# Optimization experiments

Hardware: AMD Instinct MI355X
Metric: run time of the kernel (lower is better)

## Reference

```python
import jax, jax.numpy as jnp
import numpy as np

EPS_L2 = 1e-6
EPS_RMS = 1e-6

def _dw_causal(x, w):
    # depthwise causal conv: x [B,L,C], w [C,K] (torch Conv1d weight [C,1,K] squeezed)
    K = w.shape[1]
    L = x.shape[1]
    xp = jnp.pad(x, ((0, 0), (K - 1, 0), (0, 0)))
    out = jnp.zeros_like(x)
    for j in range(K):  # K=4, fixed small kernel
        out = out + w[:, j] * xp[:, j:j + L, :]
    return out

def _qkv_conv(x, dw, pw):
    # depthwise causal conv -> pointwise 1x1 conv -> SiLU
    return jax.nn.silu(_dw_causal(x, dw) @ pw.T)

def _l2n(x):
    return x / (jnp.linalg.norm(x, axis=-1, keepdims=True) + EPS_L2)

def setup_inputs() -> dict:
    key = jax.random.key(0)
    B, L, D, M, P, K = 2, 1024, 2048, 2048, 8, 4
    ks = jax.random.split(key, 16)
    inp = {}
    inp['x'] = jax.random.normal(ks[0], (B, L, D), dtype=jnp.float32)
    inp['Wq'] = jax.random.normal(ks[1], (M, D), dtype=jnp.float32) * 0.02
    inp['Wk'] = jax.random.normal(ks[2], (M, D), dtype=jnp.float32) * 0.02
    inp['Wv'] = jax.random.normal(ks[3], (M, D), dtype=jnp.float32) * 0.02
    inp['q_dw'] = jax.random.normal(ks[4], (M, K), dtype=jnp.float32) * 0.1
    inp['k_dw'] = jax.random.normal(ks[5], (M, K), dtype=jnp.float32) * 0.1
    inp['v_dw'] = jax.random.normal(ks[6], (M, K), dtype=jnp.float32) * 0.1
    inp['q_pw'] = jax.random.normal(ks[7], (M, M), dtype=jnp.float32) * 0.02
    inp['k_pw'] = jax.random.normal(ks[8], (M, M), dtype=jnp.float32) * 0.02
    inp['v_pw'] = jax.random.normal(ks[9], (M, M), dtype=jnp.float32) * 0.02
    inp['pk'] = jax.random.normal(ks[10], (P, M), dtype=jnp.float32) * 0.02
    inp['pv'] = jax.random.normal(ks[11], (P, M), dtype=jnp.float32) * 0.02
    inp['mlp_w1'] = jnp.eye(M, dtype=jnp.float32) * 0.1
    inp['mlp_w2'] = jnp.eye(M, dtype=jnp.float32) * 0.1
    inp['eta_w'] = jnp.zeros((1, D), dtype=jnp.float32)
    inp['eta_b'] = jnp.full((1,), 2.0, dtype=jnp.float32)
    inp['theta_w'] = jnp.zeros((1, D), dtype=jnp.float32)
    inp['theta_b'] = jnp.full((1,), -1.0, dtype=jnp.float32)
    inp['alpha_w'] = jnp.zeros((1, D), dtype=jnp.float32)
    inp['alpha_b'] = jnp.full((1,), -2.0, dtype=jnp.float32)
    inp['gate_w'] = jax.random.normal(ks[12], (M, M), dtype=jnp.float32) * 0.02
    inp['gate_b'] = jnp.zeros((M,), dtype=jnp.float32)
    inp['out_w'] = jax.random.normal(ks[13], (D, M), dtype=jnp.float32) * 0.02
    inp['ln_w'] = jnp.ones((D,), dtype=jnp.float32)
    inp['mem_state'] = jnp.zeros((M, M), dtype=jnp.float32)
    inp['sur_state'] = jnp.zeros((M, M), dtype=jnp.float32)
    return inp

def reference(x, Wq, Wk, Wv, q_dw, q_pw, k_dw, k_pw, v_dw, v_pw, pk, pv,
              mlp_w1, mlp_w2, eta_w, eta_b, theta_w, theta_b, alpha_w, alpha_b,
              gate_w, gate_b, out_w, ln_w, mem_state, sur_state):
    B, L, D = x.shape
    M = Wq.shape[0]
    P = pk.shape[0]
    # projections + causal depthwise-separable convs + SiLU
    q = _qkv_conv(x @ Wq.T, q_dw, q_pw)
    k = _qkv_conv(x @ Wk.T, k_dw, k_pw)
    v = _qkv_conv(x @ Wv.T, v_dw, v_pw)
    q = _l2n(q)
    k = _l2n(k)
    # data-dependent eta/theta/alpha from mean-pooled input, scalarized
    x_pooled = x.mean(axis=1)  # [B, D]
    eta = jax.nn.sigmoid(x_pooled @ eta_w.T + eta_b).mean()
    theta = jax.nn.sigmoid(x_pooled @ theta_w.T + theta_b).mean()
    alpha = jax.nn.sigmoid(x_pooled @ alpha_w.T + alpha_b).mean()
    # persistent memory tokens
    pk_n = _l2n(pk)
    k_wp = jnp.concatenate([jnp.broadcast_to(pk_n[None], (B, P, M)), k], axis=1)
    v_wp = jnp.concatenate([jnp.broadcast_to(pv[None], (B, P, M)), v], axis=1)
    # test-time memory update (torch.no_grad block -> stop_gradient)
    pred = jnp.einsum('blm,mh->blh', k, mem_state)
    err = v - pred
    momentary = jnp.einsum('bld,blh->dh', k, err) / (B * L)
    new_surprise = eta * sur_state + theta * momentary
    new_memory = (1.0 - alpha) * mem_state + new_surprise
    snapshot = jax.lax.stop_gradient(new_memory)
    # retrieval: linear memory + deep memory MLP
    linear_ret = jnp.einsum('blm,mh->blh', q, snapshot)
    mlp_ret = jax.nn.silu(q @ mlp_w1.T) @ mlp_w2.T
    retrieved = linear_ret + mlp_ret
    # causal attention with always-visible persistent tokens
    scores = jnp.einsum('blm,bpm->blp', q, k_wp) / jnp.sqrt(jnp.float32(M))
    col = jnp.arange(P + L)
    row = jnp.arange(L)
    mask = (col[None, :] < P) | ((col[None, :] - P) <= row[:, None])  # [L, P+L]
    scores = jnp.where(mask[None], scores, -jnp.inf)
    attn = jax.nn.softmax(scores.astype(jnp.float32), axis=-1).astype(x.dtype)
    context = jnp.einsum('blp,bpm->blm', attn, v_wp)
    retrieved = retrieved + context
    # gated output projection + residual + RMSNorm
    gate = jax.nn.sigmoid(retrieved @ gate_w.T + gate_b)
    out = x + (gate * retrieved) @ out_w.T
    rms = jnp.sqrt(jnp.mean(out * out, axis=-1, keepdims=True) + EPS_RMS)
    return (out / rms) * ln_w
```

## Files before the change

kernel.cpp:

```cpp
#include <hip/hip_runtime.h>
#include <hip/hip_bf16.h>


#define NROWS 2048
#define MD    2048
#define PL    1032
#define PLP   1152
#define NM    4194304

using bf16x8 = __attribute__((ext_vector_type(8))) __bf16;
using f32x4  = __attribute__((ext_vector_type(4))) float;
using u16x8  = __attribute__((ext_vector_type(8))) unsigned short;

__device__ __forceinline__ unsigned short f2bf(float f) {
    union { float f; unsigned int u; } c; c.f = f;
    unsigned int u = c.u;
    return (unsigned short)((u + 0x7fffu + ((u >> 16) & 1u)) >> 16);
}
__device__ __forceinline__ float bf2f(unsigned short h) {
    union { float f; unsigned int u; } c; c.u = ((unsigned int)h) << 16;
    return c.f;
}
__device__ __forceinline__ float ldf(const float* p) { return *p; }
__device__ __forceinline__ float ldf(const unsigned short* p) { return bf2f(*p); }
__device__ __forceinline__ float sigm(float x) { return 1.f / (1.f + __expf(-x)); }
__device__ __forceinline__ float silu(float x) { return x / (1.f + __expf(-x)); }

__device__ __forceinline__ float block_reduce_sum(float v) {
    __shared__ float ws[4];
    #pragma unroll
    for (int o = 32; o > 0; o >>= 1) v += __shfl_down(v, o);
    __syncthreads();
    if ((threadIdx.x & 63) == 0) ws[threadIdx.x >> 6] = v;
    __syncthreads();
    return (ws[0] + ws[1]) + (ws[2] + ws[3]);
}
__device__ __forceinline__ float block_reduce_max(float v) {
    __shared__ float wm[4];
    #pragma unroll
    for (int o = 32; o > 0; o >>= 1) v = fmaxf(v, __shfl_down(v, o));
    __syncthreads();
    if ((threadIdx.x & 63) == 0) wm[threadIdx.x >> 6] = v;
    __syncthreads();
    return fmaxf(fmaxf(wm[0], wm[1]), fmaxf(wm[2], wm[3]));
}

__device__ __forceinline__ void load_lds16(const unsigned short* g, unsigned short* l) {
    __builtin_amdgcn_global_load_lds(
        (const __attribute__((address_space(1))) unsigned int*)g,
        (__attribute__((address_space(3))) unsigned int*)l, 16, 0, 0);
}
__device__ __forceinline__ void raw_barrier() {
    __asm__ volatile("" ::: "memory");
    __builtin_amdgcn_s_barrier();
    __asm__ volatile("" ::: "memory");
}
__device__ __forceinline__ void epi_store(int epi, float* Cf, unsigned short* Ch,
                                          long off, float v) {
    if (epi == 0)      Cf[off] = v;
    else if (epi == 1) Cf[off] += v;
    else if (epi == 2) Ch[off] = f2bf(v);
    else               Ch[off] = f2bf(silu(v));
}

__global__ __launch_bounds__(256) void gemm_nt(
    const unsigned short* __restrict__ A, const unsigned short* __restrict__ Bm,
    void* __restrict__ Cv, int Mc, int K, long sA, long sB, long sCb, int epiPack)
{
    __shared__ unsigned short As[2][8192];
    __shared__ unsigned short Bs[2][4096];
    const int tid = threadIdx.x, lane = tid & 63, w = tid >> 6;
    const int l16 = lane & 15, quad = lane >> 4;
    const int wr = (w >> 1) * 64, wc = (w & 1) * 32;
    const long rowBase = (long)blockIdx.y * 128;
    const long colBase = (long)blockIdx.x * 64;
    const unsigned short* Ap = A + (long)blockIdx.z * sA;
    const unsigned short* Bp = Bm + (long)blockIdx.z * sB;
    const int epi = (epiPack >> (blockIdx.z * 4)) & 15;
    const int r8 = lane >> 3;
    const int cg = (lane & 7) ^ r8;

    const unsigned short* gA[4]; const unsigned short* gB[2];
    unsigned short* lA[4]; unsigned short* lB[2];
    #pragma unroll
    for (int t = 0; t < 4; ++t) {
        int ch = w * 4 + t;
        gA[t] = Ap + (rowBase + ch * 8 + r8) * (long)K + cg * 8;
        lA[t] = &As[0][ch * 512];
    }
    #pragma unroll
    for (int t = 0; t < 2; ++t) {
        int ch = w * 2 + t;
        gB[t] = Bp + (colBase + ch * 8 + r8) * (long)K + cg * 8;
        lB[t] = &Bs[0][ch * 512];
    }

    f32x4 acc[4][2] = {};
    #pragma unroll
    for (int t = 0; t < 4; ++t) { load_lds16(gA[t], lA[t]); gA[t] += 64; }
    #pragma unroll
    for (int t = 0; t < 2; ++t) { load_lds16(gB[t], lB[t]); gB[t] += 64; }

    const int nIter = K >> 6;
    for (int it = 0; it < nIter; ++it) {
        const int cb = it & 1;
        if (it + 1 < nIter) {
            const int nb = cb ^ 1;
            #pragma unroll
            for (int t = 0; t < 4; ++t) { load_lds16(gA[t], lA[t] + nb * 8192); gA[t] += 64; }
            #pragma unroll
            for (int t = 0; t < 2; ++t) { load_lds16(gB[t], lB[t] + nb * 4096); gB[t] += 64; }
            __builtin_amdgcn_s_waitcnt(0xF76);
        } else {
            __builtin_amdgcn_s_waitcnt(0xF70);
        }
        raw_barrier();
        const unsigned short* Ac = As[cb];
        const unsigned short* Bc = Bs[cb];
        #pragma unroll
        for (int ks = 0; ks < 2; ++ks) {
            const int cl = ((ks * 4 + quad) ^ (l16 & 7)) * 8;
            bf16x8 af[4], bfr[2];
            #pragma unroll
            for (int i = 0; i < 4; ++i)
                af[i] = *(const bf16x8*)&Ac[(wr + i * 16 + l16) * 64 + cl];
            #pragma unroll
            for (int j = 0; j < 2; ++j)
                bfr[j] = *(const bf16x8*)&Bc[(wc + j * 16 + l16) * 64 + cl];
            #pragma unroll
            for (int i = 0; i < 4; ++i)
                #pragma unroll
                for (int j = 0; j < 2; ++j)
                    acc[i][j] = __builtin_amdgcn_mfma_f32_16x16x32_bf16(af[i], bfr[j], acc[i][j], 0, 0, 0);
        }
        raw_barrier();
    }

    char* Cb = (char*)Cv + (long)blockIdx.z * sCb;
    float* Cf = (float*)Cb;
    unsigned short* Ch = (unsigned short*)Cb;
    #pragma unroll
    for (int i = 0; i < 4; ++i)
        #pragma unroll
        for (int r = 0; r < 4; ++r) {
            long gr = rowBase + wr + i * 16 + quad * 4 + r;
            #pragma unroll
            for (int j = 0; j < 2; ++j) {
                long gc = colBase + wc + j * 16 + l16;
                epi_store(epi, Cf, Ch, gr * (long)Mc + gc, acc[i][j][r]);
            }
        }
}

#define G256_RD_A(p)                                                            \
    _Pragma("unroll") for (int fr = 0; fr < 2; ++fr)                            \
    _Pragma("unroll") for (int ks = 0; ks < 2; ++ks)                            \
        af[fr][ks] = *(const bf16x8*)&Ac[(wr + ((p) * 2 + fr) * 16 + l16) * 64  \
                                         + ((ks * 4 + quad) ^ (l16 & 7)) * 8];
#define G256_MFMA(p)                                                            \
    __builtin_amdgcn_s_setprio(1);                                              \
    _Pragma("unroll") for (int ks = 0; ks < 2; ++ks)                            \
    _Pragma("unroll") for (int fr = 0; fr < 2; ++fr)                            \
    _Pragma("unroll") for (int fc = 0; fc < 4; ++fc)                            \
        acc[(p) * 2 + fr][fc] = __builtin_amdgcn_mfma_f32_16x16x32_bf16(        \
            af[fr][ks], bfr[fc][ks], acc[(p) * 2 + fr][fc], 0, 0, 0);           \
    __builtin_amdgcn_s_setprio(0);
#define G256_STG_A(h)                                                           \
    do { load_lds16(gA[h][0], &Anx[lofs[h][0]]); gA[h][0] += 64;                \
         load_lds16(gA[h][1], &Anx[lofs[h][1]]); gA[h][1] += 64; } while (0)
#define G256_STG_B(h)                                                           \
    do { load_lds16(gB[h][0], &Bnx[lofs[h][0]]); gB[h][0] += 64;                \
         load_lds16(gB[h][1], &Bnx[lofs[h][1]]); gB[h][1] += 64; } while (0)

__global__ __launch_bounds__(512, 2) void gemm_nt_256(
    const unsigned short* __restrict__ A, const unsigned short* __restrict__ Bm,
    void* __restrict__ Cv, int Mc, int K, long sA, long sB, long sCb, int epiPack)
{
    __shared__ unsigned short As[2][16384];
    __shared__ unsigned short Bs[2][16384];
    const int tid = threadIdx.x, lane = tid & 63, w = tid >> 6;
    const int l16 = lane & 15, quad = lane >> 4;
    const int wr = (w >> 2) * 128, wc = (w & 3) * 64;
    const long rowBase = (long)blockIdx.y * 256;
    const long colBase = (long)blockIdx.x * 256;
    const unsigned short* Ap = A + (long)blockIdx.z * sA;
    const unsigned short* Bp = Bm + (long)blockIdx.z * sB;
    const int epi = (epiPack >> (blockIdx.z * 4)) & 15;
    const int r8 = lane >> 3;
    const int cg = (lane & 7) ^ r8;

    const unsigned short* gA[2][2]; const unsigned short* gB[2][2];
    int lofs[2][2];
    #pragma unroll
    for (int h = 0; h < 2; ++h)
        #pragma unroll
        for (int j = 0; j < 2; ++j) {
            const int rowOff = h * 128 + j * 64 + w * 8 + r8;
            gA[h][j] = Ap + (rowBase + rowOff) * (long)K + cg * 8;
            gB[h][j] = Bp + (colBase + rowOff) * (long)K + cg * 8;
            lofs[h][j] = (h * 128 + j * 64 + w * 8) * 64;
        }

    const int nT = K >> 6;
    f32x4 acc[8][4] = {};

    #pragma unroll
    for (int h = 0; h < 2; ++h)
        #pragma unroll
        for (int j = 0; j < 2; ++j) { load_lds16(gA[h][j], &As[0][lofs[h][j]]); gA[h][j] += 64; }
    #pragma unroll
    for (int h = 0; h < 2; ++h)
        #pragma unroll
        for (int j = 0; j < 2; ++j) { load_lds16(gB[h][j], &Bs[0][lofs[h][j]]); gB[h][j] += 64; }
    if (nT > 1) {
        #pragma unroll
        for (int h = 0; h < 2; ++h)
            #pragma unroll
            for (int j = 0; j < 2; ++j) { load_lds16(gB[h][j], &Bs[1][lofs[h][j]]); gB[h][j] += 64; }
        __builtin_amdgcn_s_waitcnt(0x0F74);
    } else {
        __builtin_amdgcn_s_waitcnt(0x0F70);
    }
    raw_barrier();

    for (int t = 0; t < nT; ++t) {
        const int cb = t & 1;
        const unsigned short* Ac = As[cb];
        const unsigned short* Bc = Bs[cb];
        unsigned short* Anx = As[cb ^ 1];
        unsigned short* Bnx = Bs[cb];
        const bool stA = (t + 1 < nT);
        const bool stB = (t + 2 < nT);
        bf16x8 bfr[4][2];
        bf16x8 af[2][2];

        #pragma unroll
        for (int fc = 0; fc < 4; ++fc)
            #pragma unroll
            for (int ks = 0; ks < 2; ++ks)
                bfr[fc][ks] = *(const bf16x8*)&Bc[(wc + fc * 16 + l16) * 64
                                                 + ((ks * 4 + quad) ^ (l16 & 7)) * 8];
        G256_RD_A(0)
        if (stA) G256_STG_A(0);
        raw_barrier();
        G256_MFMA(0)
        raw_barrier();

        G256_RD_A(1)
        if (stA) G256_STG_A(1);
        raw_barrier();
        G256_MFMA(1)
        raw_barrier();

        G256_RD_A(2)
        if (stB) G256_STG_B(0);
        raw_barrier();
        G256_MFMA(2)
        raw_barrier();

        G256_RD_A(3)
        if (stB) {
            G256_STG_B(1);
            __builtin_amdgcn_s_waitcnt(0x0F74);
        } else {
            __builtin_amdgcn_s_waitcnt(0x0F70);
        }
        raw_barrier();
        G256_MFMA(3)
        raw_barrier();
    }

    char* Cb = (char*)Cv + (long)blockIdx.z * sCb;
    float* Cf = (float*)Cb;
    unsigned short* Ch = (unsigned short*)Cb;
    #pragma unroll
    for (int i = 0; i < 8; ++i)
        #pragma unroll
        for (int r = 0; r < 4; ++r) {
            long gr = rowBase + wr + i * 16 + quad * 4 + r;
            #pragma unroll
            for (int j = 0; j < 4; ++j) {
                long gc = colBase + wc + j * 16 + l16;
                epi_store(epi, Cf, Ch, gr * (long)Mc + gc, acc[i][j][r]);
            }
        }
}

template <typename TS>
__global__ void k_transpose(const TS* __restrict__ src, unsigned short* __restrict__ dst,
                            int R, int C, int dstLd, int dstOff, long sSrc, long sDst)
{
    __shared__ float tile[32][33];
    const TS* sp = src + (long)blockIdx.z * sSrc;
    unsigned short* dp = dst + (long)blockIdx.z * sDst;
    int c0 = blockIdx.x * 32, r0 = blockIdx.y * 32;
    int tx = threadIdx.x, ty = threadIdx.y;
    #pragma unroll
    for (int i = 0; i < 4; ++i)
        tile[ty + i * 8][tx] = ldf(&sp[(long)(r0 + ty + i * 8) * C + c0 + tx]);
    __syncthreads();
    #pragma unroll
    for (int i = 0; i < 4; ++i)
        dp[(long)(c0 + ty + i * 8) * dstLd + dstOff + r0 + tx] = f2bf(tile[tx][ty + i * 8]);
}

__global__ void k_errT_kT(const unsigned short* __restrict__ vf, const float* __restrict__ pred,
                          const unsigned short* __restrict__ k_bf, unsigned short* __restrict__ eT)
{
    __shared__ float tile[32][33];
    int z = blockIdx.z;
    int c0 = blockIdx.x * 32, r0 = blockIdx.y * 32;
    int tx = threadIdx.x, ty = threadIdx.y;
    #pragma unroll
    for (int i = 0; i < 4; ++i) {
        long idx = (long)(r0 + ty + i * 8) * MD + c0 + tx;
        tile[ty + i * 8][tx] = (z == 0) ? (bf2f(vf[idx]) - pred[idx]) : bf2f(k_bf[idx]);
    }
    __syncthreads();
    unsigned short* dst = eT + (long)z * NM;
    #pragma unroll
    for (int i = 0; i < 4; ++i)
        dst[(long)(c0 + ty + i * 8) * MD + r0 + tx] = f2bf(tile[tx][ty + i * 8]);
}

__global__ void k_snapT(const float* __restrict__ mem, const float* __restrict__ sur,
                        const float* __restrict__ momT, const float* __restrict__ scal,
                        unsigned short* __restrict__ dst)
{
    __shared__ float tile[32][33];
    float eta = scal[0], theta = scal[1], alpha = scal[2];
    int h0 = blockIdx.y * 32, d0 = blockIdx.x * 32;
    int tx = threadIdx.x, ty = threadIdx.y;
    #pragma unroll
    for (int i = 0; i < 4; ++i) {
        long idx = (long)(d0 + ty + i * 8) * MD + h0 + tx;
        tile[ty + i * 8][tx] = (1.f - alpha) * mem[idx] + eta * sur[idx];
    }
    __syncthreads();
    #pragma unroll
    for (int i = 0; i < 4; ++i) {
        long oidx = (long)(h0 + ty + i * 8) * MD + d0 + tx;
        dst[oidx] = f2bf(tile[tx][ty + i * 8] + theta * (1.f / 2048.f) * momT[oidx]);
    }
}

__global__ void k_cvt_multi(const float* s0, const float* s1, const float* s2, const float* s3,
                            const float* s4, const float* s5, const float* s6, const float* s7,
                            unsigned short* d0, unsigned short* d1, unsigned short* d2, unsigned short* d3,
                            unsigned short* d4, unsigned short* d5, unsigned short* d6, unsigned short* d7)
{
    int seg = blockIdx.x >> 11;
    const float* s; unsigned short* d;
    switch (seg) {
        case 0: s = s0; d = d0; break;  case 1: s = s1; d = d1; break;
        case 2: s = s2; d = d2; break;  case 3: s = s3; d = d3; break;
        case 4: s = s4; d = d4; break;  case 5: s = s5; d = d5; break;
        case 6: s = s6; d = d6; break;  default: s = s7; d = d7; break;
    }
    long idx = ((long)(blockIdx.x & 2047) * 256 + threadIdx.x) * 8;
    float4 a = *(const float4*)(s + idx);
    float4 b = *(const float4*)(s + idx + 4);
    u16x8 o;
    o[0] = f2bf(a.x); o[1] = f2bf(a.y); o[2] = f2bf(a.z); o[3] = f2bf(a.w);
    o[4] = f2bf(b.x); o[5] = f2bf(b.y); o[6] = f2bf(b.z); o[7] = f2bf(b.w);
    *(u16x8*)(d + idx) = o;
}

__global__ void k_dwconv(const unsigned short* __restrict__ tproj,
                         const float* __restrict__ qdw, const float* __restrict__ kdw,
                         const float* __restrict__ vdw, unsigned short* __restrict__ conv)
{
    long u = (long)blockIdx.x * 256 + threadIdx.x;
    long flat = u * 8;
    int z = (int)(flat >> 22);
    int rem = (int)(flat & (NM - 1));
    int n = rem >> 11, m = rem & 2047;
    int l = n & 1023;
    const float* dw = (z == 0) ? qdw : (z == 1) ? kdw : vdw;
    const unsigned short* src = tproj + (long)n * 6144 + z * 2048 + m;
    float4 dwv[8];
    #pragma unroll
    for (int e = 0; e < 8; ++e) dwv[e] = *(const float4*)(dw + (m + e) * 4);
    float acc[8] = {};
    #pragma unroll
    for (int j = 0; j < 4; ++j) {
        int dl = j - 3;
        if (l + dl >= 0) {
            u16x8 r = *(const u16x8*)(src + (long)dl * 6144);
            #pragma unroll
            for (int e = 0; e < 8; ++e)
                acc[e] += ((const float*)&dwv[e])[j] * bf2f(r[e]);
        }
    }
    u16x8 o;
    #pragma unroll
    for (int e = 0; e < 8; ++e) o[e] = f2bf(acc[e]);
    *(u16x8*)(conv + (long)z * NM + (long)n * 2048 + m) = o;
}

__global__ void k_post_qkv(const float* __restrict__ t_big, unsigned short* __restrict__ q_bf,
                           unsigned short* __restrict__ k_bf, unsigned short* __restrict__ vf,
                           unsigned short* __restrict__ kwp)
{
    int bid = blockIdx.x, z = bid >> 11, n = bid & 2047;
    const float* row = t_big + (long)z * NM + (long)n * 2048;
    int t = threadIdx.x;
    float4 a = *(const float4*)(row + t * 8);
    float4 b = *(const float4*)(row + t * 8 + 4);
    float v[8] = {silu(a.x), silu(a.y), silu(a.z), silu(a.w),
                  silu(b.x), silu(b.y), silu(b.z), silu(b.w)};
    if (z == 2) {
        u16x8 o;
        #pragma unroll
        for (int e = 0; e < 8; ++e) o[e] = f2bf(v[e]);
        *(u16x8*)(vf + (long)n * 2048 + t * 8) = o;
        return;
    }
    float ss = 0.f;
    #pragma unroll
    for (int e = 0; e < 8; ++e) ss += v[e] * v[e];
    ss = block_reduce_sum(ss);
    float inv = 1.f / (sqrtf(ss) + 1e-6f);
    u16x8 o;
    #pragma unroll
    for (int e = 0; e < 8; ++e) o[e] = f2bf(v[e] * inv);
    if (z == 0) {
        *(u16x8*)(q_bf + (long)n * 2048 + t * 8) = o;
    } else {
        *(u16x8*)(k_bf + (long)n * 2048 + t * 8) = o;
        int bb = n >> 10, l = n & 1023;
        *(u16x8*)(kwp + ((long)bb * PLP + 8 + l) * MD + t * 8) = o;
    }
}

__global__ void k_misc(const float* __restrict__ pk, const float* __restrict__ pv,
                       unsigned short* __restrict__ kwp, unsigned short* __restrict__ vwpT)
{
    int bid = blockIdx.x, t = threadIdx.x;
    if (bid < 8) {
        const float* row = pk + bid * MD;
        float4 a = *(const float4*)(row + t * 8);
        float4 b = *(const float4*)(row + t * 8 + 4);
        float v[8] = {a.x, a.y, a.z, a.w, b.x, b.y, b.z, b.w};
        float ss = 0.f;
        #pragma unroll
        for (int e = 0; e < 8; ++e) ss += v[e] * v[e];
        ss = block_reduce_sum(ss);
        float inv = 1.f / (sqrtf(ss) + 1e-6f);
        u16x8 o;
        #pragma unroll
        for (int e = 0; e < 8; ++e) o[e] = f2bf(v[e] * inv);
        *(u16x8*)(kwp + (long)bid * MD + t * 8) = o;
        *(u16x8*)(kwp + (long)PLP * MD + (long)bid * MD + t * 8) = o;
    } else if (bid < 72) {
        int i = (bid - 8) * 256 + t;
        int m = i >> 3, pp = i & 7;
        unsigned short h = f2bf(pv[pp * MD + m]);
        vwpT[(long)m * PLP + pp] = h;
        vwpT[(long)MD * PLP + (long)m * PLP + pp] = h;
    } else if (bid < 312) {
        long flat = ((long)(bid - 72) * 256 + t) * 8;
        int b = (int)(flat / 245760);
        int r = (int)(flat % 245760);
        int j = 1032 + (r >> 11), m = r & 2047;
        u16x8 zz = {};
        *(u16x8*)(kwp + ((long)b * PLP + j) * MD + m) = zz;
    } else {
        long flat = ((long)(bid - 312) * 256 + t) * 8;
        int bm = (int)(flat / 120);
        int o = (int)(flat % 120);
        u16x8 zz = {};
        *(u16x8*)(vwpT + (long)bm * PLP + 1032 + o) = zz;
    }
}

__global__ void k_pooled(const float* __restrict__ x, const float* __restrict__ ew,
                         const float* __restrict__ tw, const float* __restrict__ aw,
                         float* __restrict__ dots) {
    int b = blockIdx.y;
    long base = (long)b * 1024 * MD;
    long start = (long)blockIdx.x * 8192;
    float s0 = 0, s1 = 0, s2 = 0;
    for (int s = 0; s < 32; ++s) {
        long f = start + threadIdx.x + (long)s * 256;
        float xv = x[base + f];
        int d = (int)(f & (MD - 1));
        s0 += xv * ew[d]; s1 += xv * tw[d]; s2 += xv * aw[d];
    }
    s0 = block_reduce_sum(s0);
    if (threadIdx.x == 0) atomicAdd(&dots[0 + b], s0);
    s1 = block_reduce_sum(s1);
    if (threadIdx.x == 0) atomicAdd(&dots[2 + b], s1);
    s2 = block_reduce_sum(s2);
    if (threadIdx.x == 0) atomicAdd(&dots[4 + b], s2);
}
__global__ void k_scal_fin(const float* __restrict__ dots, const float* __restrict__ eb,
                           const float* __restrict__ tb, const float* __restrict__ ab,
                           float* __restrict__ scal) {
    if (threadIdx.x == 0 && blockIdx.x == 0) {
        const float invL = 1.f / 1024.f;
        float e = 0, th = 0, al = 0;
        for (int b = 0; b < 2; ++b) {
            e  += sigm(dots[0 + b] * invL + eb[0]);
            th += sigm(dots[2 + b] * invL + tb[0]);
            al += sigm(dots[4 + b] * invL + ab[0]);
        }
        scal[0] = e * 0.5f; scal[1] = th * 0.5f; scal[2] = al * 0.5f;
    }
}

__global__ void k_addcvt(const float* __restrict__ a, const float* __restrict__ b,
                         unsigned short* __restrict__ o) {
    long i = ((long)blockIdx.x * 256 + threadIdx.x) * 8;
    float4 a0 = *(const float4*)(a + i), a1 = *(const float4*)(a + i + 4);
    float4 b0 = *(const float4*)(b + i), b1 = *(const float4*)(b + i + 4);
    u16x8 r;
    r[0] = f2bf(a0.x + b0.x); r[1] = f2bf(a0.y + b0.y); r[2] = f2bf(a0.z + b0.z); r[3] = f2bf(a0.w + b0.w);
    r[4] = f2bf(a1.x + b1.x); r[5] = f2bf(a1.y + b1.y); r[6] = f2bf(a1.z + b1.z); r[7] = f2bf(a1.w + b1.w);
    *(u16x8*)(o + i) = r;
}
__global__ void k_gate8(const float* __restrict__ pre, const float* __restrict__ gb,
                        const float* __restrict__ ret, const float* __restrict__ mlp2,
                        unsigned short* __restrict__ o) {
    long i = ((long)blockIdx.x * 256 + threadIdx.x) * 8;
    int m = (int)(i & (MD - 1));
    float4 p0 = *(const float4*)(pre + i),  p1 = *(const float4*)(pre + i + 4);
    float4 r0 = *(const float4*)(ret + i),  r1 = *(const float4*)(ret + i + 4);
    float4 q0 = *(const float4*)(mlp2 + i), q1 = *(const float4*)(mlp2 + i + 4);
    float4 g0 = *(const float4*)(gb + m),   g1 = *(const float4*)(gb + m + 4);
    u16x8 r;
    r[0] = f2bf(sigm(p0.x + g0.x) * (r0.x + q0.x));
    r[1] = f2bf(sigm(p0.y + g0.y) * (r0.y + q0.y));
    r[2] = f2bf(sigm(p0.z + g0.z) * (r0.z + q0.z));
    r[3] = f2bf(sigm(p0.w + g0.w) * (r0.w + q0.w));
    r[4] = f2bf(sigm(p1.x + g1.x) * (r1.x + q1.x));
    r[5] = f2bf(sigm(p1.y + g1.y) * (r1.y + q1.y));
    r[6] = f2bf(sigm(p1.z + g1.z) * (r1.z + q1.z));
    r[7] = f2bf(sigm(p1.w + g1.w) * (r1.w + q1.w));
    *(u16x8*)(o + i) = r;
}

__global__ void k_softmax(const float* __restrict__ S, unsigned short* __restrict__ attn) {
    int l = blockIdx.x, b = blockIdx.y;
    long base = ((long)b * 1024 + l) * PLP;
    int nvis = 8 + l + 1;
    const float scale = 0.022097086912079608f;
    int t = threadIdx.x;
    float vals[5];
    float mx = -1e30f;
    #pragma unroll
    for (int s = 0; s < 5; ++s) {
        int j = t + s * 256;
        float v = -1e30f;
        if (j < nvis) v = S[base + j] * scale;
        vals[s] = v;
        mx = fmaxf(mx, v);
    }
    mx = block_reduce_max(mx);
    float sum = 0.f;
    #pragma unroll
    for (int s = 0; s < 5; ++s) {
        int j = t + s * 256;
        float e = 0.f;
        if (j < nvis) e = __expf(vals[s] - mx);
        vals[s] = e; sum += e;
    }
    sum = block_reduce_sum(sum);
    float inv = 1.f / sum;
    #pragma unroll
    for (int s = 0; s < 5; ++s) {
        int j = t + s * 256;
        if (j < PLP) attn[base + j] = f2bf(vals[s] * inv);
    }
}

__global__ void k_final(const float* __restrict__ x, const float* __restrict__ y,
                        const float* __restrict__ lnw, float* __restrict__ out) {
    int n = blockIdx.x;
    long base = (long)n * MD;
    int t = threadIdx.x;
    float4 a0 = *(const float4*)(x + base + t * 8), a1 = *(const float4*)(x + base + t * 8 + 4);
    float4 b0 = *(const float4*)(y + base + t * 8), b1 = *(const float4*)(y + base + t * 8 + 4);
    float v[8] = {a0.x + b0.x, a0.y + b0.y, a0.z + b0.z, a0.w + b0.w,
                  a1.x + b1.x, a1.y + b1.y, a1.z + b1.z, a1.w + b1.w};
    float ss = 0.f;
    #pragma unroll
    for (int e = 0; e < 8; ++e) ss += v[e] * v[e];
    ss = block_reduce_sum(ss);
    float inv = rsqrtf(ss * (1.f / 2048.f) + 1e-6f);
    float4 w0 = *(const float4*)(lnw + t * 8), w1 = *(const float4*)(lnw + t * 8 + 4);
    float4 o0 = {v[0] * inv * w0.x, v[1] * inv * w0.y, v[2] * inv * w0.z, v[3] * inv * w0.w};
    float4 o1 = {v[4] * inv * w1.x, v[5] * inv * w1.y, v[6] * inv * w1.z, v[7] * inv * w1.w};
    *(float4*)(out + base + t * 8) = o0;
    *(float4*)(out + base + t * 8 + 4) = o1;
}

static inline void gemm64(hipStream_t st, const void* A, const void* B, void* C,
                          int Mc, int K, long sA, long sB, long sCb,
                          int gx, int gy, int gz, int epiPack) {
    hipLaunchKernelGGL(gemm_nt, dim3(gx, gy, gz), dim3(256), 0, st,
                       (const unsigned short*)A, (const unsigned short*)B, C,
                       Mc, K, sA, sB, sCb, epiPack);
}
static inline void gemm256(hipStream_t st, const void* A, const void* B, void* C,
                           int Mc, int K, long sA, long sB, long sCb,
                           int gx, int gy, int gz, int epiPack) {
    hipLaunchKernelGGL(gemm_nt_256, dim3(gx, gy, gz), dim3(512), 0, st,
                       (const unsigned short*)A, (const unsigned short*)B, C,
                       Mc, K, sA, sB, sCb, epiPack);
}

extern "C" void kernel_launch(void* const* d_in, const int* in_sizes, int n_in,
                              void* d_out, int out_size, void* d_ws, size_t ws_size,
                              hipStream_t stream) {
    const float* x    = (const float*)d_in[0];
    const float* Wq   = (const float*)d_in[1];
    const float* Wk   = (const float*)d_in[2];
    const float* Wv   = (const float*)d_in[3];
    const float* qdw  = (const float*)d_in[4];
    const float* kdw  = (const float*)d_in[5];
    const float* vdw  = (const float*)d_in[6];
    const float* qpw  = (const float*)d_in[7];
    const float* kpw  = (const float*)d_in[8];
    const float* vpw  = (const float*)d_in[9];
    const float* pk   = (const float*)d_in[10];
    const float* pv   = (const float*)d_in[11];
    const float* mw1  = (const float*)d_in[12];
    const float* mw2  = (const float*)d_in[13];
    const float* etaw = (const float*)d_in[14];
    const float* etab = (const float*)d_in[15];
    const float* thw  = (const float*)d_in[16];
    const float* thb  = (const float*)d_in[17];
    const float* alw  = (const float*)d_in[18];
    const float* alb  = (const float*)d_in[19];
    const float* gw   = (const float*)d_in[20];
    const float* gb   = (const float*)d_in[21];
    const float* ow   = (const float*)d_in[22];
    const float* lnw  = (const float*)d_in[23];
    const float* mem  = (const float*)d_in[24];
    const float* sur  = (const float*)d_in[25];
    float* out = (float*)d_out;

    char* ws = (char*)d_ws;
    const size_t MB = 1024 * 1024;
    float* dots = (float*)ws;
    float* scal = (float*)(ws + 1024);
    float*          t0f  = (float*)(ws + 4096);
    float*          t1f  = t0f + NM;
    float*          t2f  = t0f + 2 * NM;
    unsigned short* tproj = (unsigned short*)t0f;
    float*          retf = (float*)(ws + 4096 + 48 * MB);
    unsigned short* k_bf = (unsigned short*)(ws + 4096 + 64 * MB);
    unsigned short* q_bf = k_bf + NM;
    unsigned short* qc   = k_bf + 2 * NM;
    unsigned short* g_bf = k_bf;
    unsigned short* x_bf = (unsigned short*)(ws + 4096 + 88 * MB);
    unsigned short* vf   = x_bf;
    unsigned short* attn = x_bf;
    unsigned short* wQKV = (unsigned short*)(ws + 4096 + 96 * MB);
    unsigned short* conv = wQKV;
    unsigned short* kwp  = wQKV;
    unsigned short* vwpT = kwp + (long)2 * PLP * MD;
    unsigned short* wPW  = (unsigned short*)(ws + 4096 + 120 * MB);
    unsigned short* eT   = wPW;
    unsigned short* kT   = eT + NM;
    unsigned short* gw_bf = wPW;
    unsigned short* ow_bf = wPW + NM;
    unsigned short* wMem  = (unsigned short*)(ws + 4096 + 144 * MB);
    unsigned short* wMlp1 = wMem + NM;
    unsigned short* wSnap = wMem;
    unsigned short* wMlp2 = wMem + NM;

    const dim3 b256(256);
    const dim3 bT(32, 8);

    hipMemsetAsync(dots, 0, 256, stream);
    hipLaunchKernelGGL(k_pooled, dim3(256, 2), b256, 0, stream, x, etaw, thw, alw, dots);
    hipLaunchKernelGGL(k_scal_fin, dim3(1), dim3(64), 0, stream, dots, etab, thb, alb, scal);
    hipLaunchKernelGGL(k_cvt_multi, dim3(16384), b256, 0, stream,
                       x, Wq, Wk, Wv, qpw, kpw, vpw, mw1,
                       x_bf, wQKV, wQKV + NM, wQKV + 2 * (long)NM,
                       wPW, wPW + NM, wPW + 2 * (long)NM, wMlp1);
    hipLaunchKernelGGL(k_transpose<float>, dim3(64, 64, 1), bT, 0, stream,
                       mem, wMem, MD, MD, MD, 0, 0L, 0L);
    gemm256(stream, x_bf, wQKV, tproj, 6144, MD, 0, 0, 0, 24, 8, 1, 2);
    hipLaunchKernelGGL(k_dwconv, dim3(6144), b256, 0, stream, tproj, qdw, kdw, vdw, conv);
    gemm256(stream, conv, wPW, t0f, MD, MD, NM, NM, (long)NM * 4, 8, 8, 3, 0);
    hipLaunchKernelGGL(k_misc, dim3(552), b256, 0, stream, pk, pv, kwp, vwpT);
    hipLaunchKernelGGL(k_post_qkv, dim3(6144), b256, 0, stream, t0f, q_bf, k_bf, vf, kwp);
    hipLaunchKernelGGL(k_transpose<unsigned short>, dim3(64, 32, 2), bT, 0, stream,
                       vf, vwpT, 1024, MD, PLP, 8, (long)1024 * MD, (long)MD * PLP);
    gemm256(stream, k_bf, wMem, t0f, MD, MD, NM, NM,
            (long)((char*)qc - (char*)t0f), 8, 8, 2, 0x30);
    hipLaunchKernelGGL(k_errT_kT, dim3(64, 64, 2), bT, 0, stream, vf, t0f, k_bf, eT);
    gemm64(stream, eT, kT, t2f, MD, MD, 0, 0, 0, 32, 16, 1, 0);
    hipLaunchKernelGGL(k_snapT, dim3(64, 64), bT, 0, stream, mem, sur, t2f, scal, wSnap);
    hipLaunchKernelGGL(k_cvt_multi, dim3(6144), b256, 0, stream,
                       mw2, gw, ow, mw2, mw2, mw2, mw2, mw2,
                       wMlp2, gw_bf, ow_bf, wMlp2, wMlp2, wMlp2, wMlp2, wMlp2);
    gemm256(stream, q_bf, wSnap, retf, MD, MD, NM, NM,
            (long)((char*)t1f - (char*)retf), 8, 8, 2, 0);
    gemm64(stream, q_bf, kwp, t2f, PLP, MD,
           (long)1024 * MD, (long)PLP * MD, (long)1024 * PLP * 4, 18, 8, 2, 0);
    hipLaunchKernelGGL(k_softmax, dim3(1024, 2), b256, 0, stream, t2f, attn);
    gemm64(stream, attn, vwpT, retf, MD, PLP,
           (long)1024 * PLP, (long)MD * PLP, (long)1024 * MD * 4, 32, 8, 2, 0x11);
    hipLaunchKernelGGL(k_addcvt, dim3(2048), b256, 0, stream, retf, t1f, qc);
    gemm64(stream, qc, gw_bf, t0f, MD, MD, 0, 0, 0, 32, 16, 1, 0);
    hipLaunchKernelGGL(k_gate8, dim3(2048), b256, 0, stream, t0f, gb, retf, t1f, g_bf);
    gemm64(stream, g_bf, ow_bf, t0f, MD, MD, 0, 0, 0, 32, 16, 1, 0);
    hipLaunchKernelGGL(k_final, dim3(2048), b256, 0, stream, x, t0f, lnw, out);
}
```

Baseline: 816.1 us.

## Fuse elementwise epilogues into GEMMs, templatize big-tile GEMM width, swizzle block order

Several separate elementwise kernels (add-convert, gate, error subtraction, SiLU post-processing, x conversion) are folded into GEMM epilogues or the pooled reduction kernel, so intermediate fp32 buffers no longer make extra HBM round trips. The 256-wide GEMM becomes a template over the N tile (128/192/256) so grids fill the CUs better, for example 32x8 blocks instead of 24x8 for the QKV projection. Block IDs are remapped with an XCD-style swizzle to improve L2 locality. Intermediates now go to bf16 instead of fp32, which adds rounding error, and the epilogues become more complex.

```diff
diff --git a/kernel.cpp b/kernel.cpp
--- a/kernel.cpp
+++ b/kernel.cpp
@@ -55,28 +55,42 @@
     __builtin_amdgcn_s_barrier();
     __asm__ volatile("" ::: "memory");
 }
+__device__ __forceinline__ void swz_bid(int& bx, int& by, int& bz) {
+    const int gx = gridDim.x, gy = gridDim.y, gz = gridDim.z;
+    const int nwg = gx * gy * gz;
+    int id = blockIdx.x + gx * (blockIdx.y + gy * blockIdx.z);
+    if ((nwg & 7) == 0) { int c = nwg >> 3; id = (id & 7) * c + (id >> 3); }
+    bx = id % gx; id /= gx; by = id % gy; bz = id / gy;
+}
 __device__ __forceinline__ void epi_store(int epi, float* Cf, unsigned short* Ch,
-                                          long off, float v) {
+                                          long off, int gc, float v,
+                                          const float* gbp, const float* r1z,
+                                          const float* r2z, unsigned short* qhz) {
     if (epi == 0)      Cf[off] = v;
     else if (epi == 1) Cf[off] += v;
     else if (epi == 2) Ch[off] = f2bf(v);
-    else               Ch[off] = f2bf(silu(v));
+    else if (epi == 3) Ch[off] = f2bf(silu(v));
+    else if (epi == 4) Ch[off] = f2bf(sigm(v + gbp[gc]) * (r1z[off] + r2z[off]));
+    else { float r = Cf[off] + v; Cf[off] = r; qhz[off] = f2bf(r + r2z[off]); }
 }
 
 __global__ __launch_bounds__(256) void gemm_nt(
     const unsigned short* __restrict__ A, const unsigned short* __restrict__ Bm,
-    void* __restrict__ Cv, int Mc, int K, long sA, long sB, long sCb, int epiPack)
+    void* __restrict__ Cv, int Mc, int K, long sA, long sB, long sCb, int epiPack,
+    const float* __restrict__ gbp, const float* __restrict__ r1,
+    const float* __restrict__ r2, unsigned short* __restrict__ qh)
 {
     __shared__ unsigned short As[2][8192];
     __shared__ unsigned short Bs[2][4096];
+    int bxx, byy, bzz; swz_bid(bxx, byy, bzz);
     const int tid = threadIdx.x, lane = tid & 63, w = tid >> 6;
     const int l16 = lane & 15, quad = lane >> 4;
     const int wr = (w >> 1) * 64, wc = (w & 1) * 32;
-    const long rowBase = (long)blockIdx.y * 128;
-    const long colBase = (long)blockIdx.x * 64;
-    const unsigned short* Ap = A + (long)blockIdx.z * sA;
-    const unsigned short* Bp = Bm + (long)blockIdx.z * sB;
-    const int epi = (epiPack >> (blockIdx.z * 4)) & 15;
+    const long rowBase = (long)byy * 128;
+    const long colBase = (long)bxx * 64;
+    const unsigned short* Ap = A + (long)bzz * sA;
+    const unsigned short* Bp = Bm + (long)bzz * sB;
+    const int epi = (epiPack >> (bzz * 4)) & 15;
     const int r8 = lane >> 3;
     const int cg = (lane & 7) ^ r8;
 
@@ -136,9 +150,13 @@
         raw_barrier();
     }
 
-    char* Cb = (char*)Cv + (long)blockIdx.z * sCb;
+    char* Cb = (char*)Cv + (long)bzz * sCb;
     float* Cf = (float*)Cb;
     unsigned short* Ch = (unsigned short*)Cb;
+    const long zel = (long)bzz * (sCb >> 2);
+    const float* r1z = r1 + zel;
+    const float* r2z = r2 + zel;
+    unsigned short* qhz = qh + zel;
     #pragma unroll
     for (int i = 0; i < 4; ++i)
         #pragma unroll
@@ -147,77 +165,86 @@
             #pragma unroll
             for (int j = 0; j < 2; ++j) {
                 long gc = colBase + wc + j * 16 + l16;
-                epi_store(epi, Cf, Ch, gr * (long)Mc + gc, acc[i][j][r]);
+                epi_store(epi, Cf, Ch, gr * (long)Mc + gc, (int)gc, acc[i][j][r],
+                          gbp, r1z, r2z, qhz);
             }
         }
 }
 
-#define G256_RD_A(p)                                                            \
+#define P8_RD_A(p)                                                              \
     _Pragma("unroll") for (int fr = 0; fr < 2; ++fr)                            \
     _Pragma("unroll") for (int ks = 0; ks < 2; ++ks)                            \
         af[fr][ks] = *(const bf16x8*)&Ac[(wr + ((p) * 2 + fr) * 16 + l16) * 64  \
                                          + ((ks * 4 + quad) ^ (l16 & 7)) * 8];
-#define G256_MFMA(p)                                                            \
+#define P8_MFMA(p)                                                              \
     __builtin_amdgcn_s_setprio(1);                                              \
     _Pragma("unroll") for (int ks = 0; ks < 2; ++ks)                            \
     _Pragma("unroll") for (int fr = 0; fr < 2; ++fr)                            \
-    _Pragma("unroll") for (int fc = 0; fc < 4; ++fc)                            \
+    _Pragma("unroll") for (int fc = 0; fc < FC; ++fc)                           \
         acc[(p) * 2 + fr][fc] = __builtin_amdgcn_mfma_f32_16x16x32_bf16(        \
             af[fr][ks], bfr[fc][ks], acc[(p) * 2 + fr][fc], 0, 0, 0);           \
     __builtin_amdgcn_s_setprio(0);
-#define G256_STG_A(h)                                                           \
-    do { load_lds16(gA[h][0], &Anx[lofs[h][0]]); gA[h][0] += 64;                \
-         load_lds16(gA[h][1], &Anx[lofs[h][1]]); gA[h][1] += 64; } while (0)
-#define G256_STG_B(h)                                                           \
-    do { load_lds16(gB[h][0], &Bnx[lofs[h][0]]); gB[h][0] += 64;                \
-         load_lds16(gB[h][1], &Bnx[lofs[h][1]]); gB[h][1] += 64; } while (0)
-
-__global__ __launch_bounds__(512, 2) void gemm_nt_256(
+#define P8_STG_A(h)                                                             \
+    do { load_lds16(gA[h][0], &Anx[lofsA[h][0]]); gA[h][0] += 64;               \
+         load_lds16(gA[h][1], &Anx[lofsA[h][1]]); gA[h][1] += 64; } while (0)
+#define P8_STG_B(j)                                                             \
+    do { load_lds16(gB[j], &Bnx[lofsB[j]]); gB[j] += 64; } while (0)
+
+template <int BN>
+__global__ __launch_bounds__(512, 2) void gemm_nt_8p(
     const unsigned short* __restrict__ A, const unsigned short* __restrict__ Bm,
-    void* __restrict__ Cv, int Mc, int K, long sA, long sB, long sCb, int epiPack)
-{
+    void* __restrict__ Cv, int Mc, int K, long sA, long sB, long sCb, int epiPack,
+    const unsigned short* __restrict__ rh)
+{
+    constexpr int LB = BN / 64;
+    constexpr int FC = BN / 64;
+    constexpr int WN = BN / 4;
     __shared__ unsigned short As[2][16384];
-    __shared__ unsigned short Bs[2][16384];
+    __shared__ unsigned short Bs[2][BN * 64];
+    int bx, by, bz; swz_bid(bx, by, bz);
     const int tid = threadIdx.x, lane = tid & 63, w = tid >> 6;
     const int l16 = lane & 15, quad = lane >> 4;
-    const int wr = (w >> 2) * 128, wc = (w & 3) * 64;
-    const long rowBase = (long)blockIdx.y * 256;
-    const long colBase = (long)blockIdx.x * 256;
-    const unsigned short* Ap = A + (long)blockIdx.z * sA;
-    const unsigned short* Bp = Bm + (long)blockIdx.z * sB;
-    const int epi = (epiPack >> (blockIdx.z * 4)) & 15;
+    const int wr = (w >> 2) * 128, wc = (w & 3) * WN;
+    const long rowBase = (long)by * 256;
+    const long colBase = (long)bx * BN;
+    const unsigned short* Ap = A + (long)bz * sA;
+    const unsigned short* Bp = Bm + (long)bz * sB;
+    const int epi = (epiPack >> (bz * 4)) & 15;
     const int r8 = lane >> 3;
     const int cg = (lane & 7) ^ r8;
 
-    const unsigned short* gA[2][2]; const unsigned short* gB[2][2];
-    int lofs[2][2];
+    const unsigned short* gA[2][2];
+    int lofsA[2][2];
     #pragma unroll
     for (int h = 0; h < 2; ++h)
         #pragma unroll
         for (int j = 0; j < 2; ++j) {
             const int rowOff = h * 128 + j * 64 + w * 8 + r8;
             gA[h][j] = Ap + (rowBase + rowOff) * (long)K + cg * 8;
-            gB[h][j] = Bp + (colBase + rowOff) * (long)K + cg * 8;
-            lofs[h][j] = (h * 128 + j * 64 + w * 8) * 64;
-        }
+            lofsA[h][j] = (h * 128 + j * 64 + w * 8) * 64;
+        }
+    const unsigned short* gB[LB];
+    int lofsB[LB];
+    #pragma unroll
+    for (int j = 0; j < LB; ++j) {
+        const int rowOff = j * 64 + w * 8 + r8;
+        gB[j] = Bp + (colBase + rowOff) * (long)K + cg * 8;
+        lofsB[j] = (j * 64 + w * 8) * 64;
+    }
 
     const int nT = K >> 6;
-    f32x4 acc[8][4] = {};
+    f32x4 acc[8][FC] = {};
 
     #pragma unroll
     for (int h = 0; h < 2; ++h)
         #pragma unroll
-        for (int j = 0; j < 2; ++j) { load_lds16(gA[h][j], &As[0][lofs[h][j]]); gA[h][j] += 64; }
-    #pragma unroll
-    for (int h = 0; h < 2; ++h)
-        #pragma unroll
-        for (int j = 0; j < 2; ++j) { load_lds16(gB[h][j], &Bs[0][lofs[h][j]]); gB[h][j] += 64; }
+        for (int j = 0; j < 2; ++j) { load_lds16(gA[h][j], &As[0][lofsA[h][j]]); gA[h][j] += 64; }
+    #pragma unroll
+    for (int j = 0; j < LB; ++j) { load_lds16(gB[j], &Bs[0][lofsB[j]]); gB[j] += 64; }
     if (nT > 1) {
         #pragma unroll
-        for (int h = 0; h < 2; ++h)
-            #pragma unroll
-            for (int j = 0; j < 2; ++j) { load_lds16(gB[h][j], &Bs[1][lofs[h][j]]); gB[h][j] += 64; }
-        __builtin_amdgcn_s_waitcnt(0x0F74);
+        for (int j = 0; j < LB; ++j) { load_lds16(gB[j], &Bs[1][lofsB[j]]); gB[j] += 64; }
+        __builtin_amdgcn_s_waitcnt(0x0F70 | LB);
     } else {
         __builtin_amdgcn_s_waitcnt(0x0F70);
     }
@@ -231,46 +258,50 @@
         unsigned short* Bnx = Bs[cb];
         const bool stA = (t + 1 < nT);
         const bool stB = (t + 2 < nT);
-        bf16x8 bfr[4][2];
+        bf16x8 bfr[FC][2];
         bf16x8 af[2][2];
 
         #pragma unroll
-        for (int fc = 0; fc < 4; ++fc)
+        for (int fc = 0; fc < FC; ++fc)
             #pragma unroll
             for (int ks = 0; ks < 2; ++ks)
                 bfr[fc][ks] = *(const bf16x8*)&Bc[(wc + fc * 16 + l16) * 64
                                                  + ((ks * 4 + quad) ^ (l16 & 7)) * 8];
-        G256_RD_A(0)
-        if (stA) G256_STG_A(0);
-        raw_barrier();
-        G256_MFMA(0)
-        raw_barrier();
-
-        G256_RD_A(1)
-        if (stA) G256_STG_A(1);
-        raw_barrier();
-        G256_MFMA(1)
-        raw_barrier();
-
-        G256_RD_A(2)
-        if (stB) G256_STG_B(0);
-        raw_barrier();
-        G256_MFMA(2)
-        raw_barrier();
-
-        G256_RD_A(3)
+        P8_RD_A(0)
+        if (stA) P8_STG_A(0);
+        raw_barrier();
+        P8_MFMA(0)
+        raw_barrier();
+
+        P8_RD_A(1)
+        if (stA) P8_STG_A(1);
+        raw_barrier();
+        P8_MFMA(1)
+        raw_barrier();
+
+        P8_RD_A(2)
         if (stB) {
-            G256_STG_B(1);
-            __builtin_amdgcn_s_waitcnt(0x0F74);
+            #pragma unroll
+            for (int j = 0; j < (LB + 1) / 2; ++j) P8_STG_B(j);
+        }
+        raw_barrier();
+        P8_MFMA(2)
+        raw_barrier();
+
+        P8_RD_A(3)
+        if (stB) {
+            #pragma unroll
+            for (int j = (LB + 1) / 2; j < LB; ++j) P8_STG_B(j);
+            __builtin_amdgcn_s_waitcnt(0x0F70 | LB);
         } else {
             __builtin_amdgcn_s_waitcnt(0x0F70);
         }
         raw_barrier();
-        G256_MFMA(3)
-        raw_barrier();
-    }
-
-    char* Cb = (char*)Cv + (long)blockIdx.z * sCb;
+        P8_MFMA(3)
+        raw_barrier();
+    }
+
+    char* Cb = (char*)Cv + (long)bz * sCb;
     float* Cf = (float*)Cb;
     unsigned short* Ch = (unsigned short*)Cb;
     #pragma unroll
@@ -279,9 +310,14 @@
         for (int r = 0; r < 4; ++r) {
             long gr = rowBase + wr + i * 16 + quad * 4 + r;
             #pragma unroll
-            for (int j = 0; j < 4; ++j) {
+            for (int j = 0; j < FC; ++j) {
                 long gc = colBase + wc + j * 16 + l16;
-                epi_store(epi, Cf, Ch, gr * (long)Mc + gc, acc[i][j][r]);
+                long off = gr * (long)Mc + gc;
+                float v = acc[i][j][r];
+                if (epi == 0)      Cf[off] = v;
+                else if (epi == 2) Ch[off] = f2bf(v);
+                else if (epi == 3) Ch[off] = f2bf(silu(v));
+                else               Ch[off] = f2bf(bf2f(rh[off]) - v);
             }
         }
 }
@@ -304,17 +340,18 @@
         dp[(long)(c0 + ty + i * 8) * dstLd + dstOff + r0 + tx] = f2bf(tile[tx][ty + i * 8]);
 }
 
-__global__ void k_errT_kT(const unsigned short* __restrict__ vf, const float* __restrict__ pred,
+__global__ void k_errT_kT(const unsigned short* __restrict__ errN,
                           const unsigned short* __restrict__ k_bf, unsigned short* __restrict__ eT)
 {
     __shared__ float tile[32][33];
     int z = blockIdx.z;
+    const unsigned short* src = (z == 0) ? errN : k_bf;
     int c0 = blockIdx.x * 32, r0 = blockIdx.y * 32;
     int tx = threadIdx.x, ty = threadIdx.y;
     #pragma unroll
     for (int i = 0; i < 4; ++i) {
         long idx = (long)(r0 + ty + i * 8) * MD + c0 + tx;
-        tile[ty + i * 8][tx] = (z == 0) ? (bf2f(vf[idx]) - pred[idx]) : bf2f(k_bf[idx]);
+        tile[ty + i * 8][tx] = bf2f(src[idx]);
     }
     __syncthreads();
     unsigned short* dst = eT + (long)z * NM;
@@ -398,24 +435,16 @@
     *(u16x8*)(conv + (long)z * NM + (long)n * 2048 + m) = o;
 }
 
-__global__ void k_post_qkv(const float* __restrict__ t_big, unsigned short* __restrict__ q_bf,
-                           unsigned short* __restrict__ k_bf, unsigned short* __restrict__ vf,
-                           unsigned short* __restrict__ kwp)
+__global__ void k_post_qkv(const unsigned short* __restrict__ tbf, unsigned short* __restrict__ q_bf,
+                           unsigned short* __restrict__ k_bf, unsigned short* __restrict__ kwp)
 {
     int bid = blockIdx.x, z = bid >> 11, n = bid & 2047;
-    const float* row = t_big + (long)z * NM + (long)n * 2048;
+    const unsigned short* row = tbf + (long)z * NM + (long)n * 2048;
     int t = threadIdx.x;
-    float4 a = *(const float4*)(row + t * 8);
-    float4 b = *(const float4*)(row + t * 8 + 4);
-    float v[8] = {silu(a.x), silu(a.y), silu(a.z), silu(a.w),
-                  silu(b.x), silu(b.y), silu(b.z), silu(b.w)};
-    if (z == 2) {
-        u16x8 o;
-        #pragma unroll
-        for (int e = 0; e < 8; ++e) o[e] = f2bf(v[e]);
-        *(u16x8*)(vf + (long)n * 2048 + t * 8) = o;
-        return;
-    }
+    u16x8 iv = *(const u16x8*)(row + t * 8);
+    float v[8];
+    #pragma unroll
+    for (int e = 0; e < 8; ++e) v[e] = bf2f(iv[e]);
     float ss = 0.f;
     #pragma unroll
     for (int e = 0; e < 8; ++e) ss += v[e] * v[e];
@@ -476,17 +505,27 @@
 
 __global__ void k_pooled(const float* __restrict__ x, const float* __restrict__ ew,
                          const float* __restrict__ tw, const float* __restrict__ aw,
-                         float* __restrict__ dots) {
+                         float* __restrict__ dots, unsigned short* __restrict__ xbf) {
     int b = blockIdx.y;
-    long base = (long)b * 1024 * MD;
-    long start = (long)blockIdx.x * 8192;
-    float s0 = 0, s1 = 0, s2 = 0;
-    for (int s = 0; s < 32; ++s) {
-        long f = start + threadIdx.x + (long)s * 256;
-        float xv = x[base + f];
-        int d = (int)(f & (MD - 1));
-        s0 += xv * ew[d]; s1 += xv * tw[d]; s2 += xv * aw[d];
-    }
+    long flat = ((long)blockIdx.x * 256 + threadIdx.x) * 8;
+    long gi = (long)b * 1024 * MD + flat;
+    int d = (int)(flat & (MD - 1));
+    float4 a = *(const float4*)(x + gi);
+    float4 b4 = *(const float4*)(x + gi + 4);
+    float xv[8] = {a.x, a.y, a.z, a.w, b4.x, b4.y, b4.z, b4.w};
+    float4 e0 = *(const float4*)(ew + d), e1 = *(const float4*)(ew + d + 4);
+    float4 t0 = *(const float4*)(tw + d), t1 = *(const float4*)(tw + d + 4);
+    float4 w0 = *(const float4*)(aw + d), w1 = *(const float4*)(aw + d + 4);
+    u16x8 o;
+    #pragma unroll
+    for (int e = 0; e < 8; ++e) o[e] = f2bf(xv[e]);
+    *(u16x8*)(xbf + gi) = o;
+    float s0 = xv[0]*e0.x + xv[1]*e0.y + xv[2]*e0.z + xv[3]*e0.w
+             + xv[4]*e1.x + xv[5]*e1.y + xv[6]*e1.z + xv[7]*e1.w;
+    float s1 = xv[0]*t0.x + xv[1]*t0.y + xv[2]*t0.z + xv[3]*t0.w
+             + xv[4]*t1.x + xv[5]*t1.y + xv[6]*t1.z + xv[7]*t1.w;
+    float s2 = xv[0]*w0.x + xv[1]*w0.y + xv[2]*w0.z + xv[3]*w0.w
+             + xv[4]*w1.x + xv[5]*w1.y + xv[6]*w1.z + xv[7]*w1.w;
     s0 = block_reduce_sum(s0);
     if (threadIdx.x == 0) atomicAdd(&dots[0 + b], s0);
     s1 = block_reduce_sum(s1);
@@ -509,37 +548,6 @@
     }
 }
 
-__global__ void k_addcvt(const float* __restrict__ a, const float* __restrict__ b,
-                         unsigned short* __restrict__ o) {
-    long i = ((long)blockIdx.x * 256 + threadIdx.x) * 8;
-    float4 a0 = *(const float4*)(a + i), a1 = *(const float4*)(a + i + 4);
-    float4 b0 = *(const float4*)(b + i), b1 = *(const float4*)(b + i + 4);
-    u16x8 r;
-    r[0] = f2bf(a0.x + b0.x); r[1] = f2bf(a0.y + b0.y); r[2] = f2bf(a0.z + b0.z); r[3] = f2bf(a0.w + b0.w);
-    r[4] = f2bf(a1.x + b1.x); r[5] = f2bf(a1.y + b1.y); r[6] = f2bf(a1.z + b1.z); r[7] = f2bf(a1.w + b1.w);
-    *(u16x8*)(o + i) = r;
-}
-__global__ void k_gate8(const float* __restrict__ pre, const float* __restrict__ gb,
-                        const float* __restrict__ ret, const float* __restrict__ mlp2,
-                        unsigned short* __restrict__ o) {
-    long i = ((long)blockIdx.x * 256 + threadIdx.x) * 8;
-    int m = (int)(i & (MD - 1));
-    float4 p0 = *(const float4*)(pre + i),  p1 = *(const float4*)(pre + i + 4);
-    float4 r0 = *(const float4*)(ret + i),  r1 = *(const float4*)(ret + i + 4);
-    float4 q0 = *(const float4*)(mlp2 + i), q1 = *(const float4*)(mlp2 + i + 4);
-    float4 g0 = *(const float4*)(gb + m),   g1 = *(const float4*)(gb + m + 4);
-    u16x8 r;
-    r[0] = f2bf(sigm(p0.x + g0.x) * (r0.x + q0.x));
-    r[1] = f2bf(sigm(p0.y + g0.y) * (r0.y + q0.y));
-    r[2] = f2bf(sigm(p0.z + g0.z) * (r0.z + q0.z));
-    r[3] = f2bf(sigm(p0.w + g0.w) * (r0.w + q0.w));
-    r[4] = f2bf(sigm(p1.x + g1.x) * (r1.x + q1.x));
-    r[5] = f2bf(sigm(p1.y + g1.y) * (r1.y + q1.y));
-    r[6] = f2bf(sigm(p1.z + g1.z) * (r1.z + q1.z));
-    r[7] = f2bf(sigm(p1.w + g1.w) * (r1.w + q1.w));
-    *(u16x8*)(o + i) = r;
-}
-
 __global__ void k_softmax(const float* __restrict__ S, unsigned short* __restrict__ attn) {
     int l = blockIdx.x, b = blockIdx.y;
     long base = ((long)b * 1024 + l) * PLP;
@@ -597,17 +605,21 @@
 
 static inline void gemm64(hipStream_t st, const void* A, const void* B, void* C,
                           int Mc, int K, long sA, long sB, long sCb,
-                          int gx, int gy, int gz, int epiPack) {
+                          int gx, int gy, int gz, int epiPack,
+                          const float* gbp = nullptr, const float* r1 = nullptr,
+                          const float* r2 = nullptr, unsigned short* qh = nullptr) {
     hipLaunchKernelGGL(gemm_nt, dim3(gx, gy, gz), dim3(256), 0, st,
                        (const unsigned short*)A, (const unsigned short*)B, C,
-                       Mc, K, sA, sB, sCb, epiPack);
-}
-static inline void gemm256(hipStream_t st, const void* A, const void* B, void* C,
-                           int Mc, int K, long sA, long sB, long sCb,
-                           int gx, int gy, int gz, int epiPack) {
-    hipLaunchKernelGGL(gemm_nt_256, dim3(gx, gy, gz), dim3(512), 0, st,
+                       Mc, K, sA, sB, sCb, epiPack, gbp, r1, r2, qh);
+}
+template <int BN>
+static inline void gemm8p(hipStream_t st, const void* A, const void* B, void* C,
+                          int Mc, int K, long sA, long sB, long sCb,
+                          int gx, int gy, int gz, int epiPack,
+                          const unsigned short* rh = nullptr) {
+    hipLaunchKernelGGL(gemm_nt_8p<BN>, dim3(gx, gy, gz), dim3(512), 0, st,
                        (const unsigned short*)A, (const unsigned short*)B, C,
-                       Mc, K, sA, sB, sCb, epiPack);
+                       Mc, K, sA, sB, sCb, epiPack, rh);
 }
 
 extern "C" void kernel_launch(void* const* d_in, const int* in_sizes, int n_in,
@@ -649,13 +661,15 @@
     float*          t1f  = t0f + NM;
     float*          t2f  = t0f + 2 * NM;
     unsigned short* tproj = (unsigned short*)t0f;
+    unsigned short* t_bf  = (unsigned short*)t0f;
+    unsigned short* vf    = t_bf + 2 * (long)NM;
     float*          retf = (float*)(ws + 4096 + 48 * MB);
     unsigned short* k_bf = (unsigned short*)(ws + 4096 + 64 * MB);
     unsigned short* q_bf = k_bf + NM;
     unsigned short* qc   = k_bf + 2 * NM;
     unsigned short* g_bf = k_bf;
     unsigned short* x_bf = (unsigned short*)(ws + 4096 + 88 * MB);
-    unsigned short* vf   = x_bf;
+    unsigned short* errN = x_bf;
     unsigned short* attn = x_bf;
     unsigned short* wQKV = (unsigned short*)(ws + 4096 + 96 * MB);
     unsigned short* conv = wQKV;
@@ -675,39 +689,39 @@
     const dim3 bT(32, 8);
 
     hipMemsetAsync(dots, 0, 256, stream);
-    hipLaunchKernelGGL(k_pooled, dim3(256, 2), b256, 0, stream, x, etaw, thw, alw, dots);
+    hipLaunchKernelGGL(k_pooled, dim3(1024, 2), b256, 0, stream, x, etaw, thw, alw, dots, x_bf);
     hipLaunchKernelGGL(k_scal_fin, dim3(1), dim3(64), 0, stream, dots, etab, thb, alb, scal);
-    hipLaunchKernelGGL(k_cvt_multi, dim3(16384), b256, 0, stream,
-                       x, Wq, Wk, Wv, qpw, kpw, vpw, mw1,
-                       x_bf, wQKV, wQKV + NM, wQKV + 2 * (long)NM,
-                       wPW, wPW + NM, wPW + 2 * (long)NM, wMlp1);
+    hipLaunchKernelGGL(k_cvt_multi, dim3(14336), b256, 0, stream,
+                       Wq, Wk, Wv, qpw, kpw, vpw, mw1, mw1,
+                       wQKV, wQKV + NM, wQKV + 2 * (long)NM,
+                       wPW, wPW + NM, wPW + 2 * (long)NM, wMlp1, wMlp1);
     hipLaunchKernelGGL(k_transpose<float>, dim3(64, 64, 1), bT, 0, stream,
                        mem, wMem, MD, MD, MD, 0, 0L, 0L);
-    gemm256(stream, x_bf, wQKV, tproj, 6144, MD, 0, 0, 0, 24, 8, 1, 2);
+    gemm8p<192>(stream, x_bf, wQKV, tproj, 6144, MD, 0, 0, 0, 32, 8, 1, 0x2);
     hipLaunchKernelGGL(k_dwconv, dim3(6144), b256, 0, stream, tproj, qdw, kdw, vdw, conv);
-    gemm256(stream, conv, wPW, t0f, MD, MD, NM, NM, (long)NM * 4, 8, 8, 3, 0);
+    gemm8p<256>(stream, conv, wPW, t_bf, MD, MD, NM, NM, (long)NM * 2, 8, 8, 3, 0x333);
     hipLaunchKernelGGL(k_misc, dim3(552), b256, 0, stream, pk, pv, kwp, vwpT);
-    hipLaunchKernelGGL(k_post_qkv, dim3(6144), b256, 0, stream, t0f, q_bf, k_bf, vf, kwp);
+    hipLaunchKernelGGL(k_post_qkv, dim3(4096), b256, 0, stream, t_bf, q_bf, k_bf, kwp);
     hipLaunchKernelGGL(k_transpose<unsigned short>, dim3(64, 32, 2), bT, 0, stream,
                        vf, vwpT, 1024, MD, PLP, 8, (long)1024 * MD, (long)MD * PLP);
-    gemm256(stream, k_bf, wMem, t0f, MD, MD, NM, NM,
-            (long)((char*)qc - (char*)t0f), 8, 8, 2, 0x30);
-    hipLaunchKernelGGL(k_errT_kT, dim3(64, 64, 2), bT, 0, stream, vf, t0f, k_bf, eT);
+    gemm8p<128>(stream, k_bf, wMem, errN, MD, MD, NM, NM,
+                (long)((char*)qc - (char*)errN), 16, 8, 2, 0x37, vf);
+    hipLaunchKernelGGL(k_errT_kT, dim3(64, 64, 2), bT, 0, stream, errN, k_bf, eT);
     gemm64(stream, eT, kT, t2f, MD, MD, 0, 0, 0, 32, 16, 1, 0);
     hipLaunchKernelGGL(k_snapT, dim3(64, 64), bT, 0, stream, mem, sur, t2f, scal, wSnap);
     hipLaunchKernelGGL(k_cvt_multi, dim3(6144), b256, 0, stream,
                        mw2, gw, ow, mw2, mw2, mw2, mw2, mw2,
                        wMlp2, gw_bf, ow_bf, wMlp2, wMlp2, wMlp2, wMlp2, wMlp2);
-    gemm256(stream, q_bf, wSnap, retf, MD, MD, NM, NM,
-            (long)((char*)t1f - (char*)retf), 8, 8, 2, 0);
+    gemm8p<128>(stream, q_bf, wSnap, retf, MD, MD, NM, NM,
+                (long)((char*)t1f - (char*)retf), 16, 8, 2, 0x00);
     gemm64(stream, q_bf, kwp, t2f, PLP, MD,
            (long)1024 * MD, (long)PLP * MD, (long)1024 * PLP * 4, 18, 8, 2, 0);
     hipLaunchKernelGGL(k_softmax, dim3(1024, 2), b256, 0, stream, t2f, attn);
     gemm64(stream, attn, vwpT, retf, MD, PLP,
-           (long)1024 * PLP, (long)MD * PLP, (long)1024 * MD * 4, 32, 8, 2, 0x11);
-    hipLaunchKernelGGL(k_addcvt, dim3(2048), b256, 0, stream, retf, t1f, qc);
-    gemm64(stream, qc, gw_bf, t0f, MD, MD, 0, 0, 0, 32, 16, 1, 0);
-    hipLaunchKernelGGL(k_gate8, dim3(2048), b256, 0, stream, t0f, gb, retf, t1f, g_bf);
+           (long)1024 * PLP, (long)MD * PLP, (long)1024 * MD * 4, 32, 8, 2, 0x55,
+           nullptr, retf, t1f, qc);
+    gemm64(stream, qc, gw_bf, g_bf, MD, MD, 0, 0, 0, 32, 16, 1, 4,
+           gb, retf, t1f, nullptr);
     gemm64(stream, g_bf, ow_bf, t0f, MD, MD, 0, 0, 0, 32, 16, 1, 0);
     hipLaunchKernelGGL(k_final, dim3(2048), b256, 0, stream, x, t0f, lnw, out);
 }
```

Measured after the change: 860.4 us. +5.4%, slower.
